# Performance work log

Hardware: AMD Instinct MI355X
Metric: run time of the kernel (lower is better)

Reference implementation:

```python
import jax, jax.numpy as jnp
import numpy as np

NUM_GROUPS = 4194304  # 2^22 groups
GROUP_SIZE = 32
PACKED_GROUP_SIZE = GROUP_SIZE // 2 + 1  # 16 data bytes + 1 scale byte


def setup_inputs() -> dict:
    key = jax.random.key(0)
    packed = jax.random.randint(key, (NUM_GROUPS * PACKED_GROUP_SIZE,), 0, 256, dtype=jnp.int32)
    return {"packed": packed, "group_size": GROUP_SIZE, "ebits": 2, "mbits": 1}


def reference(packed, group_size, ebits, mbits):
    # MX4 -> fp32 dequantization: unpack 4-bit nibbles + per-group exp2 scale.
    packed_group_size = group_size // 2 + 1
    num_groups = packed.shape[0] // packed_group_size
    clamp_max = 2 ** (2 ** ebits - 1)                      # 8 for ebits=2
    max_val = clamp_max * (2.0 - 2.0 ** (-mbits))          # 12.0 for mbits=1

    pg = packed.reshape(num_groups, packed_group_size)
    # last byte of each group is the shared scale exponent (biased by 127)
    log_scale = jnp.clip(pg[:, -1].astype(jnp.float32) - 127.0, -126.0, 127.0)
    group_scale = jnp.exp2(log_scale)                      # (num_groups,)

    data = pg[:, : group_size // 2]                        # (num_groups, group_size//2)
    low = (data & 15).astype(jnp.float32)
    high = ((data >> 4) & 15).astype(jnp.float32)
    # interleave low/high nibbles: element order [low0, high0, low1, high1, ...]
    unpacked = jnp.stack([low, high], axis=-1).reshape(num_groups, group_size)
    unpacked = unpacked - jnp.float32(clamp_max)

    out = unpacked / jnp.float32(max_val) * group_scale[:, None]
    return out.reshape(-1).astype(jnp.float32)
```

## Files before the change

### kernel.cpp

```cpp
#include <hip/hip_runtime.h>


constexpr int kGroupSize = 32;
constexpr int kPGS = kGroupSize / 2 + 1;

__global__ __launch_bounds__(256) void dequant_mxfp4_kernel(
    const int* __restrict__ packed,
    const int* __restrict__ ebits_p,
    const int* __restrict__ mbits_p,
    float* __restrict__ out,
    int n_vec4)
{
    int tid = blockIdx.x * 256 + threadIdx.x;
    if (tid >= n_vec4) return;

    int ebits = ebits_p[0];
    int mbits = mbits_p[0];
    float clamp_max = (float)(1 << ((1 << ebits) - 1));
    float inv_max   = 1.0f / (clamp_max * (2.0f - exp2f((float)(-mbits))));

    int g  = tid >> 3;
    int b0 = (tid & 7) * 2;
    int base = g * kPGS;

    int w0 = packed[base + b0];
    int w1 = packed[base + b0 + 1];
    int s  = packed[base + kGroupSize / 2];

    int e = s - 127;
    e = min(max(e, -126), 127);
    float coef = ldexpf(1.0f, e) * inv_max;

    float4 r;
    r.x = ((float)(w0 & 15)        - clamp_max) * coef;
    r.y = ((float)((w0 >> 4) & 15) - clamp_max) * coef;
    r.z = ((float)(w1 & 15)        - clamp_max) * coef;
    r.w = ((float)((w1 >> 4) & 15) - clamp_max) * coef;

    reinterpret_cast<float4*>(out)[tid] = r;
}

extern "C" void kernel_launch(void* const* d_in, const int* in_sizes, int n_in,
                              void* d_out, int out_size, void* d_ws, size_t ws_size,
                              hipStream_t stream) {
    const int* packed  = (const int*)d_in[0];
    const int* ebits_p = (const int*)d_in[2];
    const int* mbits_p = (const int*)d_in[3];
    float* out = (float*)d_out;

    int n_vec4 = out_size / 4;
    int grid = (n_vec4 + 255) / 256;
    dequant_mxfp4_kernel<<<grid, 256, 0, stream>>>(packed, ebits_p, mbits_p, out, n_vec4);
}
```

Measured before the change: 691.1 us.

## Stage packed tiles into LDS via direct global-to-LDS loads

Each block now copies a contiguous tile of 256 packed groups into shared memory using 16-byte global_load_lds transfers, then unpacks from LDS and writes float4 outputs. This replaces the strided 4-byte global reads and the scale word that eight threads each load redundantly with fully coalesced wide loads. A separate tail kernel handles leftovers. The trade-off is added LDS use per block and possible bank conflicts from the 17-word group stride.

```diff
diff --git a/kernel.cpp b/kernel.cpp
--- a/kernel.cpp
+++ b/kernel.cpp
@@ -4,23 +4,90 @@
 constexpr int kGroupSize = 32;
 constexpr int kPGS = kGroupSize / 2 + 1;
 
-__global__ __launch_bounds__(256) void dequant_mxfp4_kernel(
+constexpr int kBlock = 256;
+constexpr int kGroupsPerBlock = 256;
+constexpr int kTileWords = kGroupsPerBlock * kPGS;
+constexpr int kVec4PerBlock = kGroupsPerBlock * kGroupSize / 4;
+constexpr int kChunkWords = 256;
+constexpr int kChunks = kTileWords / kChunkWords;
+
+__global__ __launch_bounds__(kBlock) void dequant_mxfp4_lds_kernel(
+    const int* __restrict__ packed,
+    const int* __restrict__ ebits_p,
+    const int* __restrict__ mbits_p,
+    float* __restrict__ out)
+{
+    __shared__ int tile[kTileWords];
+
+    const int t    = threadIdx.x;
+    const int wave = t >> 6;
+    const int lane = t & 63;
+
+    const int* gsrc = packed + (size_t)blockIdx.x * kTileWords;
+
+#pragma unroll
+    for (int k = 0; k < 5; ++k) {
+        const int c = k * 4 + wave;
+        if (c < kChunks) {
+            const int* g = gsrc + c * kChunkWords + lane * 4;
+            __builtin_amdgcn_global_load_lds(
+                (const __attribute__((address_space(1))) int*)g,
+                (__attribute__((address_space(3))) int*)&tile[c * kChunkWords],
+                16 , 0, 0);
+        }
+    }
+
+    const int ebits = ebits_p[0];
+    const int mbits = mbits_p[0];
+    const float clamp_max = (float)(1 << ((1 << ebits) - 1));
+    const float inv_max   = 1.0f / (clamp_max * (2.0f - exp2f((float)(-mbits))));
+
+    __syncthreads();
+
+    float4* outv = reinterpret_cast<float4*>(out) + (size_t)blockIdx.x * kVec4PerBlock;
+
+#pragma unroll
+    for (int k = 0; k < kVec4PerBlock / kBlock; ++k) {
+        const int v    = t + kBlock * k;
+        const int g    = v >> 3;
+        const int b0   = (v & 7) * 2;
+        const int base = g * kPGS;
+
+        const int w0 = tile[base + b0];
+        const int w1 = tile[base + b0 + 1];
+        const int s  = tile[base + kGroupSize / 2];
+
+        int e = s - 127;
+        e = min(max(e, -126), 127);
+        const float coef = ldexpf(1.0f, e) * inv_max;
+
+        float4 r;
+        r.x = ((float)(w0 & 15)        - clamp_max) * coef;
+        r.y = ((float)((w0 >> 4) & 15) - clamp_max) * coef;
+        r.z = ((float)(w1 & 15)        - clamp_max) * coef;
+        r.w = ((float)((w1 >> 4) & 15) - clamp_max) * coef;
+
+        outv[v] = r;
+    }
+}
+
+__global__ __launch_bounds__(256) void dequant_mxfp4_tail_kernel(
     const int* __restrict__ packed,
     const int* __restrict__ ebits_p,
     const int* __restrict__ mbits_p,
     float* __restrict__ out,
-    int n_vec4)
+    int v_begin, int n_vec4)
 {
-    int tid = blockIdx.x * 256 + threadIdx.x;
-    if (tid >= n_vec4) return;
+    int v = v_begin + blockIdx.x * 256 + threadIdx.x;
+    if (v >= n_vec4) return;
 
-    int ebits = ebits_p[0];
-    int mbits = mbits_p[0];
-    float clamp_max = (float)(1 << ((1 << ebits) - 1));
-    float inv_max   = 1.0f / (clamp_max * (2.0f - exp2f((float)(-mbits))));
+    const int ebits = ebits_p[0];
+    const int mbits = mbits_p[0];
+    const float clamp_max = (float)(1 << ((1 << ebits) - 1));
+    const float inv_max   = 1.0f / (clamp_max * (2.0f - exp2f((float)(-mbits))));
 
-    int g  = tid >> 3;
-    int b0 = (tid & 7) * 2;
+    int g  = v >> 3;
+    int b0 = (v & 7) * 2;
     int base = g * kPGS;
 
     int w0 = packed[base + b0];
@@ -37,7 +104,7 @@
     r.z = ((float)(w1 & 15)        - clamp_max) * coef;
     r.w = ((float)((w1 >> 4) & 15) - clamp_max) * coef;
 
-    reinterpret_cast<float4*>(out)[tid] = r;
+    reinterpret_cast<float4*>(out)[v] = r;
 }
 
 extern "C" void kernel_launch(void* const* d_in, const int* in_sizes, int n_in,
@@ -48,7 +115,17 @@
     const int* mbits_p = (const int*)d_in[3];
     float* out = (float*)d_out;
 
-    int n_vec4 = out_size / 4;
-    int grid = (n_vec4 + 255) / 256;
-    dequant_mxfp4_kernel<<<grid, 256, 0, stream>>>(packed, ebits_p, mbits_p, out, n_vec4);
+    const int n_vec4 = out_size / 4;
+    const int n_full = n_vec4 / kVec4PerBlock;
+    const int tail   = n_vec4 - n_full * kVec4PerBlock;
+
+    if (n_full > 0) {
+        dequant_mxfp4_lds_kernel<<<n_full, kBlock, 0, stream>>>(
+            packed, ebits_p, mbits_p, out);
+    }
+    if (tail > 0) {
+        const int tgrid = (tail + 255) / 256;
+        dequant_mxfp4_tail_kernel<<<tgrid, 256, 0, stream>>>(
+            packed, ebits_p, mbits_p, out, n_full * kVec4PerBlock, n_vec4);
+    }
 }
```

After: 699.3 us. Within noise of the previous version (+1.2%).
